# Kernel tuning notes

Hardware: AMD Instinct MI355X
Metric: run time of the kernel (lower is better)

Reference implementation:

```python
import jax, jax.numpy as jnp
import numpy as np

H, W = 40, 128
P = H * W            # image tokens
N = P                # point tokens (matches source where N == Hh*Wh)
C = 128
K = 5                # expand_num
PAD = K // 2
KK = K * K           # 25 neighbors
SPOT = 5             # spot_num
NEG = -1e8


def _l2n(x, axis):
    return x / jnp.clip(jnp.linalg.norm(x, axis=axis, keepdims=True), 1e-12)


def _patches(x, mode, cval=0.0):
    # x: (..., H, W) -> (KK, ..., H, W): KxK sliding windows in F.unfold order
    pw = [(0, 0)] * (x.ndim - 2) + [(PAD, PAD), (PAD, PAD)]
    if mode == 'edge':
        xp = jnp.pad(x, pw, mode='edge')
    else:
        xp = jnp.pad(x, pw, mode='constant', constant_values=cval)
    return jnp.stack([xp[..., i:i + H, j:j + W] for i in range(K) for j in range(K)], 0)


def _knn_idx(pts):
    # (N,3) -> (N,KK) nearest-neighbor indices (self first), as knn_points does
    d2 = jnp.sum((pts[:, None, :] - pts[None, :, :]) ** 2, -1)  # (N,N)
    _, idx = jax.lax.top_k(-d2, KK)
    return idx


def setup_inputs():
    key = jax.random.key(0)
    k1, k2, k3 = jax.random.split(key, 3)
    return {
        'im_feats_h': jax.random.normal(k1, (1, P, C), jnp.float32),
        'pc_feats_h': jax.random.normal(k2, (1, N, C), jnp.float32),
        'points_h': jax.random.normal(k3, (1, N, 3), jnp.float32),
    }


def _forward(imf, pcf, nb):
    # imf: (P,C) image features, pcf: (N,C) point features, nb: (N,KK) point knn
    # --- im_similarity_scores ---
    fmap = imf.T.reshape(C, H, W)
    pat = _patches(fmap, 'edge')                                 # (KK,C,H,W)
    sim = jnp.sum(_l2n(pat, 1) * _l2n(fmap, 0)[None], 1)         # (KK,H,W)
    sim_score = jax.nn.softmax(sim, axis=0)
    # --- pairwise_scores im->pc ---
    s = _l2n(imf, -1) @ _l2n(pcf, -1).T                          # (P,N)
    best_score = s.max(-1).reshape(H, W)
    best_index = s.argmax(-1)                                    # (P,)
    # --- im_select_score ---
    conf = _patches(best_score, 'edge')                          # (KK,H,W)
    idxg = jnp.arange(P).reshape(H, W)
    idx_pat = _patches(idxg, 'const', -1).reshape(KK, P)         # (KK,P)
    select = jnp.where(idx_pat.reshape(KK, H, W) == -1, NEG, sim_score * conf)
    # --- im_seeding ---
    sel = select.at[KK // 2].set(NEG).reshape(KK, P).T           # (P,KK)
    _, tki = jax.lax.top_k(sel, SPOT - 1)
    tki = jnp.concatenate([jnp.full((P, 1), KK // 2, tki.dtype), tki], 1)  # (P,SPOT)
    nb_pix = jnp.clip(jnp.take_along_axis(idx_pat.T, tki, 1), 0, P - 1)
    seed = best_index[nb_pix]                                    # (P,SPOT) pc idx
    # --- im_spoting: expand seeds by point knn, scatter mask, topk-reduce ---
    spot = nb[seed].reshape(P, SPOT * KK)                        # (P,125)
    m = jnp.zeros((P, N), jnp.float32).at[jnp.arange(P)[:, None], spot].set(1.0)
    spot_mask, spot_idx_redu = jax.lax.top_k(m, SPOT * KK)
    # --- pc_similarity_scores ---
    sim_pc = jax.nn.softmax(
        jnp.sum(_l2n(pcf, -1)[:, None] * _l2n(pcf[nb], -1), -1), -1)  # (N,KK)
    # --- pc branch (symmetric, source truncated) ---
    s2 = _l2n(pcf, -1) @ _l2n(imf, -1).T                         # (N,P)
    best_pc_score = s2.max(-1)
    best_pc_idx = s2.argmax(-1)
    select_pc = (sim_pc * best_pc_score[nb]).at[:, 0].set(NEG)   # exclude self
    _, tkp = jax.lax.top_k(select_pc, SPOT - 1)
    tkp = jnp.concatenate([jnp.zeros((N, 1), tkp.dtype), tkp], 1)
    pc_seed = best_pc_idx[jnp.take_along_axis(nb, tkp, 1)]       # (N,SPOT) pixel idx
    # --- pc_spoting: expand seeds in a KxK pixel window ---
    off = jnp.arange(-PAD, PAD + 1)
    r = jnp.clip(pc_seed[..., None, None] // W + off[:, None], 0, H - 1)
    c = jnp.clip(pc_seed[..., None, None] % W + off[None, :], 0, W - 1)
    spot2 = (r * W + c).reshape(N, SPOT * KK)                    # (N,125)
    m2 = jnp.zeros((N, P), jnp.float32).at[jnp.arange(N)[:, None], spot2].set(1.0)
    spot_mask_pc, spot_idx_redu_pc = jax.lax.top_k(m2, SPOT * KK)
    return (select[None], spot_mask[None], spot_idx_redu[None],
            spot_idx_redu_pc[None], spot_mask_pc[None])


def reference(im_feats_h, pc_feats_h, points_h):
    nb = _knn_idx(points_h[0])
    return _forward(im_feats_h[0], pc_feats_h[0], nb)
```

## Files before the change

### kernel.cpp

```cpp
#include <hip/hip_runtime.h>
#include <hip/hip_fp16.h>
#include <float.h>
#include <math.h>

#define HH 40
#define WW 128
#define PP 5120
#define NN 5120
#define CC 128
#define KK 25
#define SPOT 5
#define NEGV -1e8f

#define CSPL 8
#define NSEG 16
#define EPS  1e-4f
#define LOSC 2048.0f
#define RSEGS 16
#define RSEGL (NN / RSEGS)
#define NRMB ((PP + NN) / 4)

typedef _Float16 half8 __attribute__((ext_vector_type(8)));
typedef float f32x4 __attribute__((ext_vector_type(4)));

__global__ __launch_bounds__(256) void k_prep(const float* __restrict__ imf,
                                              const float* __restrict__ pcf,
                                              const float* __restrict__ pts,
                                              float* __restrict__ imn, float* __restrict__ pcn,
                                              __half* __restrict__ imh, __half* __restrict__ iml,
                                              __half* __restrict__ pch, __half* __restrict__ pcl,
                                              int* __restrict__ nb, int* __restrict__ cnt) {
    __shared__ int hist[256];
    __shared__ int wsum2[2][4];
    __shared__ int wsum[4];
    __shared__ int wmin[4];
    __shared__ int s_b, s_need, s_cntLess;
    __shared__ unsigned long long sel[32];
    int t = threadIdx.x;
    int wid = t >> 6, lane = t & 63;

    if (blockIdx.x < NRMB) {
        if (blockIdx.x == 0 && t < 4) cnt[t] = 0;
        int row = blockIdx.x * 4 + wid;
        const float* src; float* dst; __half* dh; __half* dl; int r;
        if (row < PP) { src = imf; dst = imn; dh = imh; dl = iml; r = row; }
        else          { src = pcf; dst = pcn; dh = pch; dl = pcl; r = row - PP; }
        float2 v = *(const float2*)&src[r * CC + lane * 2];
        double ss = (double)v.x * (double)v.x + (double)v.y * (double)v.y;
#pragma unroll
        for (int o = 32; o; o >>= 1) ss += __shfl_xor(ss, o);
        double inv = 1.0 / fmax(sqrt(ss), 1e-12);
        float2 o2 = make_float2((float)((double)v.x * inv), (float)((double)v.y * inv));
        *(float2*)&dst[r * CC + lane * 2] = o2;
        __half hx = __float2half_rn(o2.x), hy = __float2half_rn(o2.y);
        float rx = o2.x - __half2float(hx), ry = o2.y - __half2float(hy);
        __half2 hh; hh.x = hx; hh.y = hy;
        __half2 ll; ll.x = __float2half_rn(rx * LOSC); ll.y = __float2half_rn(ry * LOSC);
        *(__half2*)&dh[r * CC + lane * 2] = hh;
        *(__half2*)&dl[r * CC + lane * 2] = ll;
        return;
    }

    int i = blockIdx.x - NRMB;
    float px = pts[i * 3 + 0], py = pts[i * 3 + 1], pz = pts[i * 3 + 2];

    unsigned k[20];
#pragma unroll
    for (int e = 0; e < 20; ++e) {
        int j = e * 256 + t;
        float dx = __fsub_rn(px, pts[j * 3 + 0]);
        float dy = __fsub_rn(py, pts[j * 3 + 1]);
        float dz = __fsub_rn(pz, pts[j * 3 + 2]);
        float s = __fadd_rn(__fadd_rn(__fmul_rn(dx, dx), __fmul_rn(dy, dy)),
                            __fmul_rn(dz, dz));
        k[e] = __float_as_uint(s);
    }

    int need = KK;
    unsigned bpre = 0;
    for (int bit = 7; bit >= 0; --bit) {
        int c = 0;
        unsigned want = bpre << 1;
#pragma unroll
        for (int e = 0; e < 20; ++e)
            c += ((k[e] >> (24 + bit)) == want);
#pragma unroll
        for (int o = 32; o; o >>= 1) c += __shfl_xor(c, o);
        int par = bit & 1;
        if (lane == 0) wsum2[par][wid] = c;
        __syncthreads();
        int tot = wsum2[par][0] + wsum2[par][1] + wsum2[par][2] + wsum2[par][3];
        if (tot >= need) bpre = want;
        else { bpre = want | 1; need -= tot; }
    }
    unsigned prefix = bpre << 24;

    for (int l = 1; l < 4; ++l) {
        int shift = 24 - 8 * l;
        hist[t] = 0;
        __syncthreads();
        unsigned pmask = 0xFFFFFFFFu << (shift + 8);
#pragma unroll
        for (int e = 0; e < 20; ++e)
            if ((k[e] & pmask) == prefix)
                atomicAdd(&hist[(k[e] >> shift) & 255], 1);
        __syncthreads();
        int v = hist[t], c = v;
#pragma unroll
        for (int o = 1; o < 64; o <<= 1) {
            int u = __shfl_up(c, o);
            if (lane >= o) c += u;
        }
        if (lane == 63) wsum[wid] = c;
        __syncthreads();
        for (int wv = 0; wv < wid; ++wv) c += wsum[wv];
        int cex = c - v;
        if (cex < need && c >= need) { s_b = t; s_need = need - cex; }
        __syncthreads();
        prefix |= ((unsigned)s_b) << shift;
        need = s_need;
        __syncthreads();
    }

    unsigned K = prefix;
    int needK = need;

    if (t == 0) s_cntLess = 0;
    __syncthreads();
#pragma unroll
    for (int e = 0; e < 20; ++e) {
        if (k[e] < K) {
            int slot = atomicAdd(&s_cntLess, 1);
            if (slot < 32)
                sel[slot] = ((unsigned long long)k[e] << 32) | (unsigned)(e * 256 + t);
        }
    }
    __syncthreads();
    int nl = s_cntLess;

    if (t < nl) {
        unsigned long long mine = sel[t];
        int rk = 0;
        for (int s = 0; s < nl; ++s) rk += (sel[s] < mine);
        nb[i * KK + rk] = (int)(mine & 0xFFFFFFFFull);
    }

    unsigned tmask = 0;
#pragma unroll
    for (int e = 0; e < 20; ++e)
        if (k[e] == K) tmask |= 1u << e;

    for (int q = 0; q < needK; ++q) {
        int mi = tmask ? ((__ffs(tmask) - 1) * 256 + t) : 0x7fffffff;
#pragma unroll
        for (int o = 32; o; o >>= 1) mi = min(mi, __shfl_xor(mi, o));
        if (lane == 0) wmin[wid] = mi;
        __syncthreads();
        int g = min(min(wmin[0], wmin[1]), min(wmin[2], wmin[3]));
        if (t == 0) nb[i * KK + nl + q] = g;
        if ((g & 255) == t) tmask &= ~(1u << (g >> 8));
        __syncthreads();
    }
}

__global__ __launch_bounds__(256) void k_rowmax(const __half* __restrict__ imh,
                                                const __half* __restrict__ iml,
                                                const __half* __restrict__ pch,
                                                const __half* __restrict__ pcl,
                                                float* __restrict__ pval,
                                                float* __restrict__ pv2,
                                                int* __restrict__ pidx) {
    const __half* Ah = (blockIdx.z == 0) ? imh : pch;
    const __half* Al = (blockIdx.z == 0) ? iml : pcl;
    const __half* Bh = (blockIdx.z == 0) ? pch : imh;
    const __half* Bl = (blockIdx.z == 0) ? pcl : iml;
    __shared__ char sB[2 * 32768];

    int t = threadIdx.x;
    int wave = t >> 6, l = t & 63;
    int wrow = wave >> 1, wcol = wave & 1;
    int lg = l >> 4, lc = l & 15;
    int rb = blockIdx.x * 64;
    const int segLen = NN / CSPL;
    const int nCh = segLen / 64;
    int segbase = blockIdx.y * segLen;
    int srow = l >> 4;
    int sblk = l & 15;

    half8 Afh[2][4], Afl[2][4];
#pragma unroll
    for (int rt = 0; rt < 2; ++rt)
#pragma unroll
        for (int ks = 0; ks < 4; ++ks) {
            int row = rb + wrow * 32 + rt * 16 + lc;
            int ho = ks * 32 + lg * 8;
            Afh[rt][ks] = *(const half8*)&Ah[(size_t)row * CC + ho];
            Afl[rt][ks] = *(const half8*)&Al[(size_t)row * CC + ho];
        }

    float v1[2][4], v2[2][4]; int i1[2][4];
#pragma unroll
    for (int rt = 0; rt < 2; ++rt)
#pragma unroll
        for (int rg = 0; rg < 4; ++rg) { v1[rt][rg] = -1e30f; v2[rt][rg] = -1e30f; i1[rt][rg] = 0; }

    auto stage = [&](int bufsel, int chbase) {
#pragma unroll
        for (int b = 0; b < 4; ++b) {
            int rbase = wave * 16 + b * 4;
            int r = rbase + srow;
            int gblk = sblk ^ (r & 7);
            __builtin_amdgcn_global_load_lds(
                (const __attribute__((address_space(1))) void*)
                    &Bh[(size_t)(chbase + r) * CC + gblk * 8],
                (__attribute__((address_space(3))) void*)
                    (sB + bufsel * 32768 + rbase * 256),
                16, 0, 0);
            __builtin_amdgcn_global_load_lds(
                (const __attribute__((address_space(1))) void*)
                    &Bl[(size_t)(chbase + r) * CC + gblk * 8],
                (__attribute__((address_space(3))) void*)
                    (sB + bufsel * 32768 + 16384 + rbase * 256),
                16, 0, 0);
        }
    };

    stage(0, segbase);
    __syncthreads();

    int cur = 0;
    for (int c = 0; c < nCh; ++c) {
        if (c + 1 < nCh) stage(cur ^ 1, segbase + (c + 1) * 64);

        f32x4 aH[2][2], aX[2][2];
#pragma unroll
        for (int rt = 0; rt < 2; ++rt)
#pragma unroll
            for (int ct = 0; ct < 2; ++ct) {
                aH[rt][ct] = (f32x4){0.f, 0.f, 0.f, 0.f};
                aX[rt][ct] = (f32x4){0.f, 0.f, 0.f, 0.f};
            }

        const char* bufp = sB + cur * 32768;
#pragma unroll
        for (int ks = 0; ks < 4; ++ks) {
            int kb = ks * 64 + lg * 16;
            half8 bh[2], bl[2];
#pragma unroll
            for (int ct = 0; ct < 2; ++ct) {
                int row = wcol * 32 + ct * 16 + lc;
                int off = row * 256 + (kb ^ ((row & 7) << 4));
                bh[ct] = *(const half8*)(bufp + off);
                bl[ct] = *(const half8*)(bufp + 16384 + off);
            }
#pragma unroll
            for (int rt = 0; rt < 2; ++rt)
#pragma unroll
                for (int ct = 0; ct < 2; ++ct) {
                    aH[rt][ct] = __builtin_amdgcn_mfma_f32_16x16x32_f16(
                        Afh[rt][ks], bh[ct], aH[rt][ct], 0, 0, 0);
                    aX[rt][ct] = __builtin_amdgcn_mfma_f32_16x16x32_f16(
                        Afh[rt][ks], bl[ct], aX[rt][ct], 0, 0, 0);
                    aX[rt][ct] = __builtin_amdgcn_mfma_f32_16x16x32_f16(
                        Afl[rt][ks], bh[ct], aX[rt][ct], 0, 0, 0);
                }
        }

#pragma unroll
        for (int rt = 0; rt < 2; ++rt)
#pragma unroll
            for (int ct = 0; ct < 2; ++ct) {
                int col = segbase + c * 64 + wcol * 32 + ct * 16 + lc;
#pragma unroll
                for (int rg = 0; rg < 4; ++rg) {
                    float v = aH[rt][ct][rg] + aX[rt][ct][rg] * (1.0f / LOSC);
                    bool gt = v > v1[rt][rg];
                    v2[rt][rg] = gt ? v1[rt][rg] : fmaxf(v2[rt][rg], v);
                    i1[rt][rg] = gt ? col : i1[rt][rg];
                    v1[rt][rg] = gt ? v : v1[rt][rg];
                }
            }
        __syncthreads();
        cur ^= 1;
    }

#pragma unroll
    for (int rt = 0; rt < 2; ++rt)
#pragma unroll
        for (int rg = 0; rg < 4; ++rg) {
            float a1 = v1[rt][rg], a2 = v2[rt][rg]; int ai = i1[rt][rg];
#pragma unroll
            for (int o = 1; o < 16; o <<= 1) {
                float o1 = __shfl_xor(a1, o);
                float o2v = __shfl_xor(a2, o);
                int   oi = __shfl_xor(ai, o);
                if (o1 > a1) { a2 = fmaxf(a1, o2v); a1 = o1; ai = oi; }
                else         { a2 = fmaxf(a2, o1); }
            }
            if (lc == 0) {
                int seg = blockIdx.y * 2 + wcol;
                size_t o = ((size_t)blockIdx.z * NSEG + seg) * PP
                         + rb + wrow * 32 + rt * 16 + lg * 4 + rg;
                pval[o] = a1; pv2[o] = a2; pidx[o] = ai;
            }
        }
}

__global__ void k_reduce_exact(const float* __restrict__ pval, const float* __restrict__ pv2,
                               const int* __restrict__ pidx,
                               const float* __restrict__ imn, const float* __restrict__ pcn,
                               int* __restrict__ bestI, int* __restrict__ bestPI,
                               double* __restrict__ bestSd, double* __restrict__ bestPSd,
                               int* __restrict__ list2, int* __restrict__ cnt) {
    int wid = threadIdx.x >> 6, lane = threadIdx.x & 63;
    int row = blockIdx.x * 4 + wid;
    int side = (row >= PP) ? 1 : 0;
    int r = side ? (row - PP) : row;
    size_t base = (size_t)side * NSEG * PP + r;

    float v1 = -1e30f, v2 = -1e30f; int i1 = 0x7fffffff;
    if (lane < NSEG) {
        v1 = pval[base + (size_t)lane * PP];
        v2 = pv2[base + (size_t)lane * PP];
        i1 = pidx[base + (size_t)lane * PP];
    }
#pragma unroll
    for (int o = 1; o < 16; o <<= 1) {
        float o1 = __shfl_xor(v1, o);
        float o2v = __shfl_xor(v2, o);
        int   oi = __shfl_xor(i1, o);
        if (o1 > v1) { v2 = fmaxf(v1, o2v); v1 = o1; i1 = oi; }
        else         { v2 = fmaxf(v2, o1); }
    }
    int bi = __shfl(i1, 0);
    float b1 = __shfl(v1, 0), b2 = __shfl(v2, 0);

    const float* A = side ? pcn : imn;
    const float* B = side ? imn : pcn;
    float2 av = *(const float2*)&A[(size_t)r * CC + lane * 2];
    float2 bv = *(const float2*)&B[(size_t)bi * CC + lane * 2];
    double s = (double)av.x * (double)bv.x + (double)av.y * (double)bv.y;
#pragma unroll
    for (int o = 32; o; o >>= 1) s += __shfl_xor(s, o);

    if (lane == 0) {
        if (side == 0) { bestI[r] = bi; bestSd[r] = s; }
        else           { bestPI[r] = bi; bestPSd[r] = s; }
        if (b1 - b2 < EPS) {
            int slot = atomicAdd(&cnt[0], 1);
            list2[slot] = r | (side << 16);
        }
    }
}

__global__ void k_recheck64a(const float* __restrict__ imn, const float* __restrict__ pcn,
                             const int* __restrict__ list2, const int* __restrict__ cnt,
                             double* __restrict__ rqv, int* __restrict__ rqi) {
    __shared__ double ad[CC];
    __shared__ double rv[4];
    __shared__ int    ri[4];
    int seg = blockIdx.x, t = threadIdx.x;
    int wid = t >> 6, lane = t & 63;
    int total = cnt[0];
    for (int e = blockIdx.y; e < total; e += gridDim.y) {
        __syncthreads();
        int ent = list2[e];
        int r = ent & 0xffff, side = ent >> 16;
        const float* Arow = (side == 0 ? imn : pcn) + (size_t)r * CC;
        const float* B    = (side == 0 ? pcn : imn);
        if (t < CC) ad[t] = (double)Arow[t];
        __syncthreads();
        double bv = -1e300; int bi = 0x7fffffff;
        for (int j = seg * RSEGL + t; j < (seg + 1) * RSEGL; j += 256) {
            double s0 = 0.0, s1 = 0.0, s2 = 0.0, s3 = 0.0;
#pragma unroll 8
            for (int c4 = 0; c4 < CC / 4; ++c4) {
                float4 b = *(const float4*)&B[(size_t)j * CC + c4 * 4];
                s0 += ad[c4 * 4 + 0] * (double)b.x;
                s1 += ad[c4 * 4 + 1] * (double)b.y;
                s2 += ad[c4 * 4 + 2] * (double)b.z;
                s3 += ad[c4 * 4 + 3] * (double)b.w;
            }
            double s = (s0 + s1) + (s2 + s3);
            if (s > bv || (s == bv && j < bi)) { bv = s; bi = j; }
        }
#pragma unroll
        for (int o = 32; o; o >>= 1) {
            double ov = __shfl_xor(bv, o); int oi = __shfl_xor(bi, o);
            if (ov > bv || (ov == bv && oi < bi)) { bv = ov; bi = oi; }
        }
        if (lane == 0) { rv[wid] = bv; ri[wid] = bi; }
        __syncthreads();
        if (t == 0) {
            for (int wv = 1; wv < 4; ++wv)
                if (rv[wv] > bv || (rv[wv] == bv && ri[wv] < bi)) { bv = rv[wv]; bi = ri[wv]; }
            rqv[(size_t)e * RSEGS + seg] = bv;
            rqi[(size_t)e * RSEGS + seg] = bi;
        }
        __syncthreads();
    }
}

__global__ void k_recheck64b(const int* __restrict__ list2, const int* __restrict__ cnt,
                             const double* __restrict__ rqv, const int* __restrict__ rqi,
                             double* __restrict__ bestSd, int* __restrict__ bestI,
                             double* __restrict__ bestPSd, int* __restrict__ bestPI) {
    int e = blockIdx.x * 256 + threadIdx.x;
    if (e >= cnt[0]) return;
    double bv = rqv[(size_t)e * RSEGS]; int bi = rqi[(size_t)e * RSEGS];
#pragma unroll 4
    for (int s = 1; s < RSEGS; ++s) {
        double ov = rqv[(size_t)e * RSEGS + s]; int oi = rqi[(size_t)e * RSEGS + s];
        if (ov > bv || (ov == bv && oi < bi)) { bv = ov; bi = oi; }
    }
    int ent = list2[e];
    int r = ent & 0xffff, side = ent >> 16;
    if (side == 0) { bestSd[r] = bv; bestI[r] = bi; }
    else           { bestPSd[r] = bv; bestPI[r] = bi; }
}

__device__ __forceinline__ void compact_bits_par(const unsigned* bits,
                                                 float* __restrict__ sm,
                                                 float* __restrict__ si, int lane) {
    unsigned w0 = bits[lane];
    unsigned w1 = bits[64 + lane];
    unsigned w2 = (lane < 32) ? bits[128 + lane] : 0u;
    int c0 = __popc(w0), c1 = __popc(w1), c2 = __popc(w2);
    int s0 = c0, s1 = c1, s2 = c2;
#pragma unroll
    for (int o = 1; o < 64; o <<= 1) {
        int u0 = __shfl_up(s0, o); if (lane >= o) s0 += u0;
        int u1 = __shfl_up(s1, o); if (lane >= o) s1 += u1;
        int u2 = __shfl_up(s2, o); if (lane >= o) s2 += u2;
    }
    int tot0 = __shfl(s0, 63);
    int tot1 = __shfl(s1, 63);
    int tot2 = __shfl(s2, 31);
    int nl = tot0 + tot1 + tot2;
    int e0 = s0 - c0;
    int e1 = tot0 + (s1 - c1);
    int e2 = tot0 + tot1 + (s2 - c2);

    {
        int base = e0; unsigned word = w0; int wi = lane;
        while (word) { int pos = __ffs(word) - 1;
            si[base] = (float)(wi * 32 + pos); sm[base] = 1.0f; word &= word - 1; ++base; }
        base = e1; word = w1; wi = 64 + lane;
        while (word) { int pos = __ffs(word) - 1;
            si[base] = (float)(wi * 32 + pos); sm[base] = 1.0f; word &= word - 1; ++base; }
        if (lane < 32) {
            base = e2; word = w2; wi = 128 + lane;
            while (word) { int pos = __ffs(word) - 1;
                si[base] = (float)(wi * 32 + pos); sm[base] = 1.0f; word &= word - 1; ++base; }
        }
    }
    {
        int wi = lane; int base = nl + 32 * wi - e0; unsigned word = ~w0;
        while (word && base < 125) { int pos = __ffs(word) - 1;
            si[base] = (float)(wi * 32 + pos); sm[base] = 0.0f; word &= word - 1; ++base; }
        wi = 64 + lane; base = nl + 32 * wi - e1; word = ~w1;
        while (word && base < 125) { int pos = __ffs(word) - 1;
            si[base] = (float)(wi * 32 + pos); sm[base] = 0.0f; word &= word - 1; ++base; }
        if (lane < 32) {
            wi = 128 + lane; base = nl + 32 * wi - e2; word = ~w2;
            while (word && base < 125) { int pos = __ffs(word) - 1;
                si[base] = (float)(wi * 32 + pos); sm[base] = 0.0f; word &= word - 1; ++base; }
        }
    }
}

__global__ void k_select_spot(const float* __restrict__ imn, const float* __restrict__ pcn,
                              const int* __restrict__ nb,
                              const double* __restrict__ bestSd, const int* __restrict__ bestI,
                              const double* __restrict__ bestPSd, const int* __restrict__ bestPI,
                              float* __restrict__ outSelect,
                              float* __restrict__ outMask, float* __restrict__ outIdx,
                              float* __restrict__ outMaskPc, float* __restrict__ outIdxPc) {
    __shared__ unsigned bits[4][160];
    __shared__ float smv[4][125];
    __shared__ float siv[4][125];
    int t = threadIdx.x;
    int wid = t >> 6, lane = t & 63;
    int bid = blockIdx.x;

    if (bid < PP / 4) {
        int pb = (bid & 7) * (PP / 4 / 8) + (bid >> 3);
        int p = pb * 4 + wid;
        int h = p >> 7, w = p & 127;

        double mysim = -1e300;
        if (lane < KK) {
            int di = lane / 5 - 2, dj = lane % 5 - 2;
            int hc = min(max(h + di, 0), HH - 1);
            int wc = min(max(w + dj, 0), WW - 1);
            const float* crow = &imn[(size_t)p * CC];
            const float* nrow = &imn[(size_t)(hc * WW + wc) * CC];
            double s0 = 0.0, s1 = 0.0, s2 = 0.0, s3 = 0.0;
#pragma unroll 8
            for (int c = 0; c < CC; c += 4) {
                float4 cv = *(const float4*)&crow[c];
                float4 nv = *(const float4*)&nrow[c];
                s0 += (double)cv.x * (double)nv.x;
                s1 += (double)cv.y * (double)nv.y;
                s2 += (double)cv.z * (double)nv.z;
                s3 += (double)cv.w * (double)nv.w;
            }
            mysim = (s0 + s1) + (s2 + s3);
        }
        double mx = mysim;
#pragma unroll
        for (int o = 1; o < 64; o <<= 1) mx = fmax(mx, __shfl_xor(mx, o));

        double e = 0.0;
        if (lane < KK) e = exp(mysim - mx);
        double sum = e;
#pragma unroll
        for (int o = 32; o; o >>= 1) sum += __shfl_xor(sum, o);
        double inv = 1.0 / sum;

        double selv = -1e300;
        if (lane < KK) {
            int di = lane / 5 - 2, dj = lane % 5 - 2;
            int h2 = h + di, w2 = w + dj;
            bool valid = (h2 >= 0 && h2 < HH && w2 >= 0 && w2 < WW);
            int hc = min(max(h2, 0), HH - 1), wc = min(max(w2, 0), WW - 1);
            double conf = bestSd[hc * WW + wc];
            double so = valid ? (e * inv * conf) : (double)NEGV;
            outSelect[lane * PP + p] = (float)so;
            selv = (lane == 12) ? (double)NEGV : so;
        }

        int tks[5]; tks[0] = 12;
        double sv = selv; int sk = (lane < KK) ? lane : 63;
#pragma unroll
        for (int s = 0; s < 4; ++s) {
            double bv = sv; int bk = sk;
#pragma unroll
            for (int o = 1; o < 64; o <<= 1) {
                double ov = __shfl_xor(bv, o);
                int ok = __shfl_xor(bk, o);
                if (ov > bv || (ov == bv && ok < bk)) { bv = ov; bk = ok; }
            }
            tks[s + 1] = bk;
            if (sk == bk) sv = -1e300;
        }

        int sd0, sd1, sd2, sd3, sd4;
#pragma unroll
        for (int s = 0; s < 5; ++s) {
            int k = tks[s];
            int di = k / 5 - 2, dj = k % 5 - 2;
            int h2 = h + di, w2 = w + dj;
            int pix = (h2 >= 0 && h2 < HH && w2 >= 0 && w2 < WW) ? (h2 * WW + w2) : -1;
            pix = min(max(pix, 0), PP - 1);
            int sd = bestI[pix];
            if (s == 0) sd0 = sd; else if (s == 1) sd1 = sd;
            else if (s == 2) sd2 = sd; else if (s == 3) sd3 = sd; else sd4 = sd;
        }

        for (int w2 = lane; w2 < 160; w2 += 64) bits[wid][w2] = 0u;
        __syncthreads();
        for (int e2 = lane; e2 < 125; e2 += 64) {
            int q = e2 / 25;
            int sd = (q == 0) ? sd0 : (q == 1) ? sd1 : (q == 2) ? sd2 : (q == 3) ? sd3 : sd4;
            int pt = nb[sd * KK + (e2 % 25)];
            atomicOr(&bits[wid][pt >> 5], 1u << (pt & 31));
        }
        __syncthreads();
        compact_bits_par(bits[wid], smv[wid], siv[wid], lane);
        for (int e2 = lane; e2 < 125; e2 += 64) {
            outMask[p * 125 + e2] = smv[wid][e2];
            outIdx[p * 125 + e2]  = siv[wid][e2];
        }
    } else {
        int bid2 = bid - PP / 4;
        int ib = (bid2 & 7) * (PP / 4 / 8) + (bid2 >> 3);
        int i = ib * 4 + wid;

        double mysim = -1e300;
        if (lane < KK) {
            int nbs = nb[i * KK + lane];
            const float* crow = &pcn[(size_t)i * CC];
            const float* nrow = &pcn[(size_t)nbs * CC];
            double s0 = 0.0, s1 = 0.0, s2 = 0.0, s3 = 0.0;
#pragma unroll 8
            for (int c = 0; c < CC; c += 4) {
                float4 cv = *(const float4*)&crow[c];
                float4 nv = *(const float4*)&nrow[c];
                s0 += (double)cv.x * (double)nv.x;
                s1 += (double)cv.y * (double)nv.y;
                s2 += (double)cv.z * (double)nv.z;
                s3 += (double)cv.w * (double)nv.w;
            }
            mysim = (s0 + s1) + (s2 + s3);
        }
        double mx = mysim;
#pragma unroll
        for (int o = 1; o < 64; o <<= 1) mx = fmax(mx, __shfl_xor(mx, o));

        double e = 0.0;
        if (lane < KK) e = exp(mysim - mx);
        double sum = e;
#pragma unroll
        for (int o = 32; o; o >>= 1) sum += __shfl_xor(sum, o);
        double inv = 1.0 / sum;

        double selv = -1e300;
        if (lane < KK)
            selv = (lane == 0) ? (double)NEGV : (e * inv * bestPSd[nb[i * KK + lane]]);

        int tks[5]; tks[0] = 0;
        double sv = selv; int sk = (lane < KK) ? lane : 63;
#pragma unroll
        for (int s = 0; s < 4; ++s) {
            double bv = sv; int bk = sk;
#pragma unroll
            for (int o = 1; o < 64; o <<= 1) {
                double ov = __shfl_xor(bv, o);
                int ok = __shfl_xor(bk, o);
                if (ov > bv || (ov == bv && ok < bk)) { bv = ov; bk = ok; }
            }
            tks[s + 1] = bk;
            if (sk == bk) sv = -1e300;
        }

        int sd0, sd1, sd2, sd3, sd4;
#pragma unroll
        for (int s = 0; s < 5; ++s) {
            int nbs = nb[i * KK + tks[s]];
            int sd = bestPI[nbs];
            if (s == 0) sd0 = sd; else if (s == 1) sd1 = sd;
            else if (s == 2) sd2 = sd; else if (s == 3) sd3 = sd; else sd4 = sd;
        }

        for (int w2 = lane; w2 < 160; w2 += 64) bits[wid][w2] = 0u;
        __syncthreads();
        for (int e2 = lane; e2 < 125; e2 += 64) {
            int q = e2 / 25;
            int sd = (q == 0) ? sd0 : (q == 1) ? sd1 : (q == 2) ? sd2 : (q == 3) ? sd3 : sd4;
            int kk = e2 % 25;
            int r0 = sd >> 7, c0 = sd & 127;
            int r = min(max(r0 + kk / 5 - 2, 0), HH - 1);
            int c = min(max(c0 + kk % 5 - 2, 0), WW - 1);
            int pix = r * WW + c;
            atomicOr(&bits[wid][pix >> 5], 1u << (pix & 31));
        }
        __syncthreads();
        compact_bits_par(bits[wid], smv[wid], siv[wid], lane);
        for (int e2 = lane; e2 < 125; e2 += 64) {
            outMaskPc[i * 125 + e2] = smv[wid][e2];
            outIdxPc[i * 125 + e2]  = siv[wid][e2];
        }
    }
}

extern "C" void kernel_launch(void* const* d_in, const int* in_sizes, int n_in,
                              void* d_out, int out_size, void* d_ws, size_t ws_size,
                              hipStream_t stream) {
    const float* imf = (const float*)d_in[0];
    const float* pcf = (const float*)d_in[1];
    const float* pts = (const float*)d_in[2];
    float* out = (float*)d_out;

    char* w = (char*)d_ws;
    double* bestSd  = (double*)w;  w += (size_t)PP * 8;
    double* bestPSd = (double*)w;  w += (size_t)NN * 8;
    double* rqv     = (double*)w;  w += (size_t)(PP + NN) * RSEGS * 8;
    float*  imn     = (float*)w;   w += (size_t)PP * CC * 4;
    float*  pcn     = (float*)w;   w += (size_t)NN * CC * 4;
    __half* imh     = (__half*)w;  w += (size_t)PP * CC * 2;
    __half* iml     = (__half*)w;  w += (size_t)PP * CC * 2;
    __half* pch     = (__half*)w;  w += (size_t)NN * CC * 2;
    __half* pcl     = (__half*)w;  w += (size_t)NN * CC * 2;
    float*  pval    = (float*)w;   w += (size_t)2 * NSEG * PP * 4;
    float*  pv2     = (float*)w;   w += (size_t)2 * NSEG * PP * 4;
    int*    pidx    = (int*)w;     w += (size_t)2 * NSEG * PP * 4;
    int*    rqi     = (int*)w;     w += (size_t)(PP + NN) * RSEGS * 4;
    int*    nb      = (int*)w;     w += (size_t)NN * KK * 4;
    int*    bestI   = (int*)w;     w += (size_t)PP * 4;
    int*    bestPI  = (int*)w;     w += (size_t)NN * 4;
    int*    list2   = (int*)w;     w += (size_t)(PP + NN) * 4;
    int*    cnt     = (int*)w;     w += 256;

    float* outSelect = out;
    float* outMask   = out + KK * PP;
    float* outIdx    = outMask + PP * 125;
    float* outIdxPc  = outIdx + PP * 125;
    float* outMaskPc = outIdxPc + NN * 125;

    k_prep<<<NRMB + NN, 256, 0, stream>>>(imf, pcf, pts, imn, pcn,
                                          imh, iml, pch, pcl, nb, cnt);
    k_rowmax<<<dim3(PP / 64, CSPL, 2), 256, 0, stream>>>(imh, iml, pch, pcl,
                                                         pval, pv2, pidx);
    k_reduce_exact<<<(PP + NN) / 4, 256, 0, stream>>>(pval, pv2, pidx, imn, pcn,
                                                      bestI, bestPI, bestSd, bestPSd,
                                                      list2, cnt);
    k_recheck64a<<<dim3(RSEGS, 256), 256, 0, stream>>>(imn, pcn, list2, cnt, rqv, rqi);
    k_recheck64b<<<(PP + NN) / 256, 256, 0, stream>>>(list2, cnt, rqv, rqi,
                                                      bestSd, bestI, bestPSd, bestPI);
    k_select_spot<<<2 * PP / 4, 256, 0, stream>>>(imn, pcn, nb, bestSd, bestI,
                                                  bestPSd, bestPI, outSelect,
                                                  outMask, outIdx, outMaskPc, outIdxPc);
}
```

Baseline: 175.3 us.

## Compute both row and column maxima from a single similarity GEMM pass

The similarity GEMM was run twice, once for image-to-point and once for point-to-image. Now only the image-to-point product is computed, and each block also reduces column-wise top-2 values and indices into per-row-tile partials. The reduce kernel then merges 80 column partials per point. This halves the MFMA work but adds per-chunk shuffles, shared-memory exchanges and larger partial buffers.

```diff
diff --git a/kernel.cpp b/kernel.cpp
--- a/kernel.cpp
+++ b/kernel.cpp
@@ -14,6 +14,7 @@
 
 #define CSPL 8
 #define NSEG 16
+#define NRT (PP / 64)
 #define EPS  1e-4f
 #define LOSC 2048.0f
 #define RSEGS 16
@@ -169,12 +170,18 @@
                                                 const __half* __restrict__ pcl,
                                                 float* __restrict__ pval,
                                                 float* __restrict__ pv2,
-                                                int* __restrict__ pidx) {
-    const __half* Ah = (blockIdx.z == 0) ? imh : pch;
-    const __half* Al = (blockIdx.z == 0) ? iml : pcl;
-    const __half* Bh = (blockIdx.z == 0) ? pch : imh;
-    const __half* Bl = (blockIdx.z == 0) ? pcl : iml;
+                                                int* __restrict__ pidx,
+                                                float* __restrict__ pvalT,
+                                                float* __restrict__ pv2T,
+                                                int* __restrict__ pidxT) {
+    const __half* Ah = imh;
+    const __half* Al = iml;
+    const __half* Bh = pch;
+    const __half* Bl = pcl;
     __shared__ char sB[2 * 32768];
+    __shared__ float sCv1[2][4][2][16];
+    __shared__ float sCv2[2][4][2][16];
+    __shared__ int   sCi [2][4][2][16];
 
     int t = threadIdx.x;
     int wave = t >> 6, l = t & 63;
@@ -266,6 +273,8 @@
                 }
         }
 
+        float cv1[2] = {-1e30f, -1e30f}, cv2[2] = {-1e30f, -1e30f};
+        int   ci1[2] = {0, 0};
 #pragma unroll
         for (int rt = 0; rt < 2; ++rt)
 #pragma unroll
@@ -278,9 +287,52 @@
                     v2[rt][rg] = gt ? v1[rt][rg] : fmaxf(v2[rt][rg], v);
                     i1[rt][rg] = gt ? col : i1[rt][rg];
                     v1[rt][rg] = gt ? v : v1[rt][rg];
+                    int grow = rb + wrow * 32 + rt * 16 + lg * 4 + rg;
+                    bool cgt = v > cv1[ct];
+                    cv2[ct] = cgt ? cv1[ct] : fmaxf(cv2[ct], v);
+                    ci1[ct] = cgt ? grow : ci1[ct];
+                    cv1[ct] = cgt ? v : cv1[ct];
                 }
             }
-        __syncthreads();
+#pragma unroll
+        for (int ct = 0; ct < 2; ++ct) {
+#pragma unroll
+            for (int o = 16; o < 64; o <<= 1) {
+                float o1 = __shfl_xor(cv1[ct], o);
+                float o2v = __shfl_xor(cv2[ct], o);
+                int   oi = __shfl_xor(ci1[ct], o);
+                if (o1 > cv1[ct]) { cv2[ct] = fmaxf(cv1[ct], o2v); cv1[ct] = o1; ci1[ct] = oi; }
+                else              { cv2[ct] = fmaxf(cv2[ct], o1); }
+            }
+        }
+        int par = c & 1;
+        if (lg == 0) {
+#pragma unroll
+            for (int ct = 0; ct < 2; ++ct) {
+                sCv1[par][wave][ct][lc] = cv1[ct];
+                sCv2[par][wave][ct][lc] = cv2[ct];
+                sCi [par][wave][ct][lc] = ci1[ct];
+            }
+        }
+        __syncthreads();
+
+        if (wrow == 0 && lg == 0) {
+#pragma unroll
+            for (int ct = 0; ct < 2; ++ct) {
+                float a1 = sCv1[par][wave][ct][lc];
+                float a2 = sCv2[par][wave][ct][lc];
+                int   ai = sCi [par][wave][ct][lc];
+                float b1 = sCv1[par][wave + 2][ct][lc];
+                float b2 = sCv2[par][wave + 2][ct][lc];
+                int   bi = sCi [par][wave + 2][ct][lc];
+                float m1, m2; int mi;
+                if (b1 > a1) { m1 = b1; mi = bi; m2 = fmaxf(a1, b2); }
+                else         { m1 = a1; mi = ai; m2 = fmaxf(a2, b1); }
+                int col = segbase + c * 64 + wcol * 32 + ct * 16 + lc;
+                size_t o = (size_t)blockIdx.x * NN + col;
+                pvalT[o] = m1; pv2T[o] = m2; pidxT[o] = mi;
+            }
+        }
         cur ^= 1;
     }
 
@@ -299,7 +351,7 @@
             }
             if (lc == 0) {
                 int seg = blockIdx.y * 2 + wcol;
-                size_t o = ((size_t)blockIdx.z * NSEG + seg) * PP
+                size_t o = (size_t)seg * PP
                          + rb + wrow * 32 + rt * 16 + lg * 4 + rg;
                 pval[o] = a1; pv2[o] = a2; pidx[o] = ai;
             }
@@ -308,6 +360,8 @@
 
 __global__ void k_reduce_exact(const float* __restrict__ pval, const float* __restrict__ pv2,
                                const int* __restrict__ pidx,
+                               const float* __restrict__ pvalT, const float* __restrict__ pv2T,
+                               const int* __restrict__ pidxT,
                                const float* __restrict__ imn, const float* __restrict__ pcn,
                                int* __restrict__ bestI, int* __restrict__ bestPI,
                                double* __restrict__ bestSd, double* __restrict__ bestPSd,
@@ -316,16 +370,28 @@
     int row = blockIdx.x * 4 + wid;
     int side = (row >= PP) ? 1 : 0;
     int r = side ? (row - PP) : row;
-    size_t base = (size_t)side * NSEG * PP + r;
 
     float v1 = -1e30f, v2 = -1e30f; int i1 = 0x7fffffff;
-    if (lane < NSEG) {
-        v1 = pval[base + (size_t)lane * PP];
-        v2 = pv2[base + (size_t)lane * PP];
-        i1 = pidx[base + (size_t)lane * PP];
-    }
-#pragma unroll
-    for (int o = 1; o < 16; o <<= 1) {
+    if (side == 0) {
+        if (lane < NSEG) {
+            v1 = pval[(size_t)lane * PP + r];
+            v2 = pv2[(size_t)lane * PP + r];
+            i1 = pidx[(size_t)lane * PP + r];
+        }
+    } else {
+        v1 = pvalT[(size_t)lane * NN + r];
+        v2 = pv2T[(size_t)lane * NN + r];
+        i1 = pidxT[(size_t)lane * NN + r];
+        if (lane < NRT - 64) {
+            float o1 = pvalT[(size_t)(64 + lane) * NN + r];
+            float o2v = pv2T[(size_t)(64 + lane) * NN + r];
+            int   oi = pidxT[(size_t)(64 + lane) * NN + r];
+            if (o1 > v1) { v2 = fmaxf(v1, o2v); v1 = o1; i1 = oi; }
+            else         { v2 = fmaxf(v2, o1); }
+        }
+    }
+#pragma unroll
+    for (int o = 1; o < 64; o <<= 1) {
         float o1 = __shfl_xor(v1, o);
         float o2v = __shfl_xor(v2, o);
         int   oi = __shfl_xor(i1, o);
@@ -672,9 +738,12 @@
     __half* iml     = (__half*)w;  w += (size_t)PP * CC * 2;
     __half* pch     = (__half*)w;  w += (size_t)NN * CC * 2;
     __half* pcl     = (__half*)w;  w += (size_t)NN * CC * 2;
-    float*  pval    = (float*)w;   w += (size_t)2 * NSEG * PP * 4;
-    float*  pv2     = (float*)w;   w += (size_t)2 * NSEG * PP * 4;
-    int*    pidx    = (int*)w;     w += (size_t)2 * NSEG * PP * 4;
+    float*  pval    = (float*)w;   w += (size_t)NSEG * PP * 4;
+    float*  pv2     = (float*)w;   w += (size_t)NSEG * PP * 4;
+    int*    pidx    = (int*)w;     w += (size_t)NSEG * PP * 4;
+    float*  pvalT   = (float*)w;   w += (size_t)NRT * NN * 4;
+    float*  pv2T    = (float*)w;   w += (size_t)NRT * NN * 4;
+    int*    pidxT   = (int*)w;     w += (size_t)NRT * NN * 4;
     int*    rqi     = (int*)w;     w += (size_t)(PP + NN) * RSEGS * 4;
     int*    nb      = (int*)w;     w += (size_t)NN * KK * 4;
     int*    bestI   = (int*)w;     w += (size_t)PP * 4;
@@ -690,9 +759,11 @@
 
     k_prep<<<NRMB + NN, 256, 0, stream>>>(imf, pcf, pts, imn, pcn,
                                           imh, iml, pch, pcl, nb, cnt);
-    k_rowmax<<<dim3(PP / 64, CSPL, 2), 256, 0, stream>>>(imh, iml, pch, pcl,
-                                                         pval, pv2, pidx);
-    k_reduce_exact<<<(PP + NN) / 4, 256, 0, stream>>>(pval, pv2, pidx, imn, pcn,
+    k_rowmax<<<dim3(NRT, CSPL, 1), 256, 0, stream>>>(imh, iml, pch, pcl,
+                                                     pval, pv2, pidx,
+                                                     pvalT, pv2T, pidxT);
+    k_reduce_exact<<<(PP + NN) / 4, 256, 0, stream>>>(pval, pv2, pidx,
+                                                      pvalT, pv2T, pidxT, imn, pcn,
                                                       bestI, bestPI, bestSd, bestPSd,
                                                       list2, cnt);
     k_recheck64a<<<dim3(RSEGS, 256), 256, 0, stream>>>(imn, pcn, list2, cnt, rqv, rqi);
```

Result: slower. 183.3 us (+4.6%).
